# Performance work log

Measured on AMD Instinct MI355X. Metric: run time of the kernel, lower is better.

Reference implementation:

```python
import jax, jax.numpy as jnp
import numpy as np

T, N, M, B = 512, 512, 256, 256

def setup_inputs() -> dict:
    key = jax.random.key(0)
    ks = jax.random.split(key, 6)
    h_t = jax.random.normal(ks[0], (1, B, M), dtype=jnp.float32)
    s_t = jax.random.normal(ks[1], (1, B, M), dtype=jnp.float32)
    data = jax.random.normal(ks[2], (B, T, N), dtype=jnp.float32)
    # torch Linear weight layout: (out_features, in_features)
    W_e = jax.random.normal(ks[3], (T, 2 * M), dtype=jnp.float32) / np.sqrt(2 * M)
    U_e = jax.random.normal(ks[4], (T, T), dtype=jnp.float32) / np.sqrt(T)
    v_e = jax.random.normal(ks[5], (1, T), dtype=jnp.float32) / np.sqrt(T)
    return {"h_t": h_t, "s_t": s_t, "data": data, "W_e": W_e, "U_e": U_e, "v_e": v_e}

def reference(h_t, s_t, data, W_e, U_e, v_e):
    # h_t, s_t: (1, B, m) -> (B, 2m); query is identical across the n repeats,
    # so project once and broadcast instead of materializing (B, n, 2m).
    query = jnp.concatenate([h_t[0], s_t[0]], axis=-1)          # (B, 2m)
    wq = query @ W_e.T                                          # (B, T)
    ud = jnp.einsum('btn,st->bns', data, U_e)                   # (B, n, T)
    alpha = jnp.tanh(wq[:, None, :] + ud)                       # (B, n, T)
    scores = jnp.einsum('bnt,t->bn', alpha, v_e[0])             # (B, n)
    attn = jax.nn.softmax(scores, axis=-1)[:, None, :]          # (B, 1, n)
    return attn
```

## Files before the change

### kernel.cpp

```cpp
#include <hip/hip_runtime.h>
#include <hip/hip_bf16.h>
#include <cmath>

#define T_DIM 512
#define N_DIM 512
#define M_DIM 256
#define B_DIM 256

typedef __bf16 bf16x8 __attribute__((ext_vector_type(8)));
typedef float  f32x4  __attribute__((ext_vector_type(4)));
typedef unsigned int u32;

__device__ __forceinline__ void gload16(const __bf16* g, __bf16* l) {
    __builtin_amdgcn_global_load_lds(
        (const __attribute__((address_space(1))) void*)g,
        (__attribute__((address_space(3))) void*)l, 16, 0, 0);
}

__device__ __forceinline__ int bkey(int r) { return ((r >> 3) ^ (r >> 1)) & 3; }

__device__ __forceinline__ float ftanh(float x) {
    return 1.f - 2.f / (__expf(2.f * x) + 1.f);
}

__global__ __launch_bounds__(256) void uconv_kernel(
    const float* __restrict__ U, __bf16* __restrict__ Uh)
{
    const int i = (blockIdx.x * 256 + threadIdx.x) * 2;
    float2 v = *(const float2*)(U + i);
    Uh[i]   = (__bf16)v.x;
    Uh[i+1] = (__bf16)v.y;
}

__global__ __launch_bounds__(256) void wq_kernel(
    const float* __restrict__ h_t, const float* __restrict__ s_t,
    const float* __restrict__ W_e, float* __restrict__ wq)
{
    __shared__ float q[2 * M_DIM];
    const int b = blockIdx.x;
    const int tid = threadIdx.x;
    q[tid]         = h_t[(size_t)b * M_DIM + tid];
    q[M_DIM + tid] = s_t[(size_t)b * M_DIM + tid];
    __syncthreads();
    for (int tt = tid; tt < T_DIM; tt += 256) {
        const float4* wrow = (const float4*)(W_e + (size_t)tt * (2 * M_DIM));
        float acc = 0.f;
        #pragma unroll 4
        for (int k4 = 0; k4 < (2 * M_DIM) / 4; ++k4) {
            float4 w = wrow[k4];
            acc += q[4*k4+0] * w.x + q[4*k4+1] * w.y
                 + q[4*k4+2] * w.z + q[4*k4+3] * w.w;
        }
        wq[(size_t)b * T_DIM + tt] = acc;
    }
}

__global__ __launch_bounds__(256, 2) void fused8_kernel(
    const float* __restrict__ data, const __bf16* __restrict__ Uh,
    const float* __restrict__ v_e, const float* __restrict__ wq,
    float* __restrict__ partial)
{
    __shared__ __align__(16) __bf16 As[2][128 * 32];
    __shared__ __align__(16) __bf16 Bs[2][256 * 32];
    __shared__ float sc[128];

    const int wg    = blockIdx.x;
    const int xcd   = wg & 7;
    const int local = wg >> 3;
    const int sh    = local & 1;
    const int q     = xcd + 8 * (local >> 1);
    const int bgrp  = q >> 2;
    const int nb    = q & 3;

    const int tid  = threadIdx.x;
    const int lane = tid & 63;
    const int wid  = tid >> 6;
    const int wm   = wid >> 1;
    const int wn   = wid & 1;

    if (tid < 128) sc[tid] = 0.f;

    f32x4 acc[4][8];
    const f32x4 zero = {0.f, 0.f, 0.f, 0.f};
    #pragma unroll
    for (int i = 0; i < 4; ++i)
        #pragma unroll
        for (int j = 0; j < 8; ++j)
            acc[i][j] = zero;

    const int rp = tid >> 4;
    const int cg = tid & 15;
    const int n0 = cg * 8;

    const float* Apan = data + ((size_t)bgrp * 4 * T_DIM) * N_DIM + nb * 128 + n0;

    const __bf16* Bb = Uh + (size_t)(sh * 256) * T_DIM;
    const int r0   = tid >> 2;
    const int keyB = bkey(r0);
    const int ce   = (((tid & 3) ^ keyB) * 8);

    const int fr = lane & 15;
    const int kb = (lane >> 4) * 8;

    int aoff[4];
    #pragma unroll
    for (int mi = 0; mi < 4; ++mi) {
        const int row = wm * 64 + mi * 16 + fr;
        aoff[mi] = row * 32 + (kb ^ (bkey(row) << 3));
    }
    int boff[8];
    #pragma unroll
    for (int ni = 0; ni < 8; ++ni) {
        const int row = wn * 128 + ni * 16 + fr;
        boff[ni] = row * 32 + (kb ^ (bkey(row) << 3));
    }

    float vev[8];
    #pragma unroll
    for (int ni = 0; ni < 8; ++ni)
        vev[ni] = v_e[sh * 256 + wn * 128 + ni * 16 + fr];
    const int g = lane >> 4;

    float4 pa0, pa1, pa2, pa3;
    {
        const float* s0 = Apan + (size_t)(2 * rp) * N_DIM;
        pa0 = *(const float4*)s0;
        pa1 = *(const float4*)(s0 + 4);
        pa2 = *(const float4*)(s0 + N_DIM);
        pa3 = *(const float4*)(s0 + N_DIM + 4);
    }
    #pragma unroll
    for (int i = 0; i < 4; ++i)
        gload16(Bb + (size_t)(i * 64 + r0) * T_DIM + ce, &Bs[0][tid * 8] + i * 64 * 32);
    {
        u32* As32 = (u32*)As[0];
        const float lo_[8] = {pa0.x, pa0.y, pa0.z, pa0.w, pa1.x, pa1.y, pa1.z, pa1.w};
        const float hi_[8] = {pa2.x, pa2.y, pa2.z, pa2.w, pa3.x, pa3.y, pa3.z, pa3.w};
        #pragma unroll
        for (int j = 0; j < 8; ++j) {
            __bf16 l = (__bf16)lo_[j];
            __bf16 h = (__bf16)hi_[j];
            u32 w = ((u32)__builtin_bit_cast(unsigned short, h) << 16)
                  |  (u32)__builtin_bit_cast(unsigned short, l);
            const int key = (cg ^ (j >> 1)) & 3;
            As32[(n0 + j) * 16 + (rp ^ (key << 2))] = w;
        }
    }
    {
        const float* sn = Apan + (size_t)(32 + 2 * rp) * N_DIM;
        pa0 = *(const float4*)sn;
        pa1 = *(const float4*)(sn + 4);
        pa2 = *(const float4*)(sn + N_DIM);
        pa3 = *(const float4*)(sn + N_DIM + 4);
    }
    __syncthreads();

    for (int t = 0; t < 64; ++t) {
        const int cur = t & 1;

        bf16x8 a[4], bv[8];
        #pragma unroll
        for (int mi = 0; mi < 4; ++mi)
            a[mi] = *(const bf16x8*)&As[cur][aoff[mi]];
        #pragma unroll
        for (int ni = 0; ni < 8; ++ni)
            bv[ni] = *(const bf16x8*)&Bs[cur][boff[ni]];

        if (t < 63) {
            const int nxt = cur ^ 1;
            const int kcol = ((t + 1) & 15) << 5;
            #pragma unroll
            for (int i = 0; i < 4; ++i)
                gload16(Bb + (size_t)(i * 64 + r0) * T_DIM + kcol + ce,
                        &Bs[nxt][tid * 8] + i * 64 * 32);
            u32* As32 = (u32*)As[nxt];
            const float lo_[8] = {pa0.x, pa0.y, pa0.z, pa0.w, pa1.x, pa1.y, pa1.z, pa1.w};
            const float hi_[8] = {pa2.x, pa2.y, pa2.z, pa2.w, pa3.x, pa3.y, pa3.z, pa3.w};
            #pragma unroll
            for (int j = 0; j < 8; ++j) {
                __bf16 l = (__bf16)lo_[j];
                __bf16 h = (__bf16)hi_[j];
                u32 w = ((u32)__builtin_bit_cast(unsigned short, h) << 16)
                      |  (u32)__builtin_bit_cast(unsigned short, l);
                const int key = (cg ^ (j >> 1)) & 3;
                As32[(n0 + j) * 16 + (rp ^ (key << 2))] = w;
            }
            if (t < 62) {
                const float* sn = Apan + (size_t)(32 * (t + 2) + 2 * rp) * N_DIM;
                pa0 = *(const float4*)sn;
                pa1 = *(const float4*)(sn + 4);
                pa2 = *(const float4*)(sn + N_DIM);
                pa3 = *(const float4*)(sn + N_DIM + 4);
            }
        }

        __builtin_amdgcn_s_setprio(1);
        #pragma unroll
        for (int mi = 0; mi < 4; ++mi)
            #pragma unroll
            for (int ni = 0; ni < 8; ++ni)
                acc[mi][ni] = __builtin_amdgcn_mfma_f32_16x16x32_bf16(a[mi], bv[ni], acc[mi][ni], 0, 0, 0);
        __builtin_amdgcn_s_setprio(0);

        __syncthreads();

        if ((t & 15) == 15) {
            const int b = bgrp * 4 + (t >> 4);
            float wqv[8];
            #pragma unroll
            for (int ni = 0; ni < 8; ++ni)
                wqv[ni] = wq[(size_t)b * T_DIM + sh * 256 + wn * 128 + ni * 16 + fr];
            #pragma unroll
            for (int mi = 0; mi < 4; ++mi) {
                #pragma unroll
                for (int rg = 0; rg < 4; ++rg) {
                    float part = 0.f;
                    #pragma unroll
                    for (int ni = 0; ni < 8; ++ni)
                        part += vev[ni] * ftanh(wqv[ni] + acc[mi][ni][rg]);
                    part += __shfl_xor(part, 1);
                    part += __shfl_xor(part, 2);
                    part += __shfl_xor(part, 4);
                    part += __shfl_xor(part, 8);
                    if (fr == 0)
                        atomicAdd(&sc[wm * 64 + mi * 16 + 4 * g + rg], part);
                }
            }
            __syncthreads();
            if (tid < 128)
                partial[((size_t)b * 2 + sh) * N_DIM + nb * 128 + tid] = sc[tid];
            if (t < 63) {
                if (tid < 128) sc[tid] = 0.f;
                #pragma unroll
                for (int i = 0; i < 4; ++i)
                    #pragma unroll
                    for (int j = 0; j < 8; ++j)
                        acc[i][j] = zero;
            }
        }
    }
}

__global__ __launch_bounds__(512) void softmax_kernel(
    const float* __restrict__ partial, float* __restrict__ out)
{
    const int b = blockIdx.x;
    const int n = threadIdx.x;
    const float* p = partial + (size_t)b * 2 * N_DIM;
    float s = p[n] + p[N_DIM + n];

    float m = s;
    #pragma unroll
    for (int off = 1; off < 64; off <<= 1)
        m = fmaxf(m, __shfl_xor(m, off));
    __shared__ float red[8];
    const int wv = n >> 6;
    if ((n & 63) == 0) red[wv] = m;
    __syncthreads();
    float bm = red[0];
    #pragma unroll
    for (int i = 1; i < 8; ++i) bm = fmaxf(bm, red[i]);

    float e = expf(s - bm);
    float t = e;
    #pragma unroll
    for (int off = 1; off < 64; off <<= 1)
        t += __shfl_xor(t, off);
    __syncthreads();
    if ((n & 63) == 0) red[wv] = t;
    __syncthreads();
    float tot = 0.f;
    #pragma unroll
    for (int i = 0; i < 8; ++i) tot += red[i];

    out[(size_t)b * N_DIM + n] = e / tot;
}

extern "C" void kernel_launch(void* const* d_in, const int* in_sizes, int n_in,
                              void* d_out, int out_size, void* d_ws, size_t ws_size,
                              hipStream_t stream) {
    const float* h_t  = (const float*)d_in[0];
    const float* s_t  = (const float*)d_in[1];
    const float* data = (const float*)d_in[2];
    const float* W_e  = (const float*)d_in[3];
    const float* U_e  = (const float*)d_in[4];
    const float* v_e  = (const float*)d_in[5];
    float* out = (float*)d_out;

    const size_t wq_elems      = (size_t)B_DIM * T_DIM;
    const size_t partial_elems = (size_t)B_DIM * 2 * N_DIM;
    const size_t u_elems       = (size_t)T_DIM * T_DIM;

    float* wq      = (float*)d_ws;
    float* partial = wq + wq_elems;
    __bf16* Uh     = (__bf16*)(partial + partial_elems);

    wq_kernel<<<B_DIM, 256, 0, stream>>>(h_t, s_t, W_e, wq);
    uconv_kernel<<<(int)(u_elems / 512), 256, 0, stream>>>(U_e, Uh);
    fused8_kernel<<<512, 256, 0, stream>>>(data, Uh, v_e, wq, partial);
    softmax_kernel<<<B_DIM, 512, 0, stream>>>(partial, out);
}
```

Measured before the change: 164.7 us.

## Merge T-halves into one 512-thread block to load each data tile once

Each block now computes all 512 T columns with 8 waves instead of splitting T across two blocks, so each data tile is read from global memory and converted to bf16 only once. Per-wave score partials go to separate shared slots and are summed without atomics, and the softmax reads a single score row. In exchange the grid is halved to 256 blocks and LDS use per block doubles, which lowers the number of waves available to hide latency.

After: 163.5 us. About the same (-0.7%).

```diff
diff --git a/kernel.cpp b/kernel.cpp
--- a/kernel.cpp
+++ b/kernel.cpp
@@ -55,30 +55,24 @@
     }
 }
 
-__global__ __launch_bounds__(256, 2) void fused8_kernel(
+__global__ __launch_bounds__(512, 2) void fused9_kernel(
     const float* __restrict__ data, const __bf16* __restrict__ Uh,
     const float* __restrict__ v_e, const float* __restrict__ wq,
-    float* __restrict__ partial)
+    float* __restrict__ scores)
 {
     __shared__ __align__(16) __bf16 As[2][128 * 32];
-    __shared__ __align__(16) __bf16 Bs[2][256 * 32];
-    __shared__ float sc[128];
-
-    const int wg    = blockIdx.x;
-    const int xcd   = wg & 7;
-    const int local = wg >> 3;
-    const int sh    = local & 1;
-    const int q     = xcd + 8 * (local >> 1);
-    const int bgrp  = q >> 2;
-    const int nb    = q & 3;
+    __shared__ __align__(16) __bf16 Bs[2][512 * 32];
+    __shared__ float sc2[4][128];
+
+    const int wg   = blockIdx.x;
+    const int bgrp = wg >> 2;
+    const int nb   = wg & 3;
 
     const int tid  = threadIdx.x;
     const int lane = tid & 63;
     const int wid  = tid >> 6;
-    const int wm   = wid >> 1;
-    const int wn   = wid & 1;
-
-    if (tid < 128) sc[tid] = 0.f;
+    const int wm   = wid >> 2;
+    const int wn   = wid & 3;
 
     f32x4 acc[4][8];
     const f32x4 zero = {0.f, 0.f, 0.f, 0.f};
@@ -88,13 +82,13 @@
         for (int j = 0; j < 8; ++j)
             acc[i][j] = zero;
 
-    const int rp = tid >> 4;
-    const int cg = tid & 15;
-    const int n0 = cg * 8;
+    const int rp = tid >> 5;
+    const int nq = tid & 31;
+    const int n0 = nq * 4;
 
     const float* Apan = data + ((size_t)bgrp * 4 * T_DIM) * N_DIM + nb * 128 + n0;
 
-    const __bf16* Bb = Uh + (size_t)(sh * 256) * T_DIM;
+    const __bf16* Bb = Uh;
     const int r0   = tid >> 2;
     const int keyB = bkey(r0);
     const int ce   = (((tid & 3) ^ keyB) * 8);
@@ -118,40 +112,37 @@
     float vev[8];
     #pragma unroll
     for (int ni = 0; ni < 8; ++ni)
-        vev[ni] = v_e[sh * 256 + wn * 128 + ni * 16 + fr];
+        vev[ni] = v_e[wn * 128 + ni * 16 + fr];
     const int g = lane >> 4;
 
-    float4 pa0, pa1, pa2, pa3;
+    float4 pa0, pa1;
     {
         const float* s0 = Apan + (size_t)(2 * rp) * N_DIM;
         pa0 = *(const float4*)s0;
-        pa1 = *(const float4*)(s0 + 4);
-        pa2 = *(const float4*)(s0 + N_DIM);
-        pa3 = *(const float4*)(s0 + N_DIM + 4);
+        pa1 = *(const float4*)(s0 + N_DIM);
     }
     #pragma unroll
     for (int i = 0; i < 4; ++i)
-        gload16(Bb + (size_t)(i * 64 + r0) * T_DIM + ce, &Bs[0][tid * 8] + i * 64 * 32);
+        gload16(Bb + (size_t)(i * 128 + r0) * T_DIM + ce,
+                &Bs[0][0] + (size_t)i * 128 * 32 + tid * 8);
     {
         u32* As32 = (u32*)As[0];
-        const float lo_[8] = {pa0.x, pa0.y, pa0.z, pa0.w, pa1.x, pa1.y, pa1.z, pa1.w};
-        const float hi_[8] = {pa2.x, pa2.y, pa2.z, pa2.w, pa3.x, pa3.y, pa3.z, pa3.w};
-        #pragma unroll
-        for (int j = 0; j < 8; ++j) {
+        const float lo_[4] = {pa0.x, pa0.y, pa0.z, pa0.w};
+        const float hi_[4] = {pa1.x, pa1.y, pa1.z, pa1.w};
+        #pragma unroll
+        for (int j = 0; j < 4; ++j) {
             __bf16 l = (__bf16)lo_[j];
             __bf16 h = (__bf16)hi_[j];
             u32 w = ((u32)__builtin_bit_cast(unsigned short, h) << 16)
                   |  (u32)__builtin_bit_cast(unsigned short, l);
-            const int key = (cg ^ (j >> 1)) & 3;
+            const int key = bkey(n0 + j);
             As32[(n0 + j) * 16 + (rp ^ (key << 2))] = w;
         }
     }
     {
         const float* sn = Apan + (size_t)(32 + 2 * rp) * N_DIM;
         pa0 = *(const float4*)sn;
-        pa1 = *(const float4*)(sn + 4);
-        pa2 = *(const float4*)(sn + N_DIM);
-        pa3 = *(const float4*)(sn + N_DIM + 4);
+        pa1 = *(const float4*)(sn + N_DIM);
     }
     __syncthreads();
 
@@ -171,26 +162,24 @@
             const int kcol = ((t + 1) & 15) << 5;
             #pragma unroll
             for (int i = 0; i < 4; ++i)
-                gload16(Bb + (size_t)(i * 64 + r0) * T_DIM + kcol + ce,
-                        &Bs[nxt][tid * 8] + i * 64 * 32);
+                gload16(Bb + (size_t)(i * 128 + r0) * T_DIM + kcol + ce,
+                        &Bs[nxt][0] + (size_t)i * 128 * 32 + tid * 8);
             u32* As32 = (u32*)As[nxt];
-            const float lo_[8] = {pa0.x, pa0.y, pa0.z, pa0.w, pa1.x, pa1.y, pa1.z, pa1.w};
-            const float hi_[8] = {pa2.x, pa2.y, pa2.z, pa2.w, pa3.x, pa3.y, pa3.z, pa3.w};
-            #pragma unroll
-            for (int j = 0; j < 8; ++j) {
+            const float lo_[4] = {pa0.x, pa0.y, pa0.z, pa0.w};
+            const float hi_[4] = {pa1.x, pa1.y, pa1.z, pa1.w};
+            #pragma unroll
+            for (int j = 0; j < 4; ++j) {
                 __bf16 l = (__bf16)lo_[j];
                 __bf16 h = (__bf16)hi_[j];
                 u32 w = ((u32)__builtin_bit_cast(unsigned short, h) << 16)
                       |  (u32)__builtin_bit_cast(unsigned short, l);
-                const int key = (cg ^ (j >> 1)) & 3;
+                const int key = bkey(n0 + j);
                 As32[(n0 + j) * 16 + (rp ^ (key << 2))] = w;
             }
             if (t < 62) {
                 const float* sn = Apan + (size_t)(32 * (t + 2) + 2 * rp) * N_DIM;
                 pa0 = *(const float4*)sn;
-                pa1 = *(const float4*)(sn + 4);
-                pa2 = *(const float4*)(sn + N_DIM);
-                pa3 = *(const float4*)(sn + N_DIM + 4);
+                pa1 = *(const float4*)(sn + N_DIM);
             }
         }
 
@@ -209,7 +198,7 @@
             float wqv[8];
             #pragma unroll
             for (int ni = 0; ni < 8; ++ni)
-                wqv[ni] = wq[(size_t)b * T_DIM + sh * 256 + wn * 128 + ni * 16 + fr];
+                wqv[ni] = wq[(size_t)b * T_DIM + wn * 128 + ni * 16 + fr];
             #pragma unroll
             for (int mi = 0; mi < 4; ++mi) {
                 #pragma unroll
@@ -223,14 +212,15 @@
                     part += __shfl_xor(part, 4);
                     part += __shfl_xor(part, 8);
                     if (fr == 0)
-                        atomicAdd(&sc[wm * 64 + mi * 16 + 4 * g + rg], part);
+                        sc2[wn][wm * 64 + mi * 16 + 4 * g + rg] = part;
                 }
             }
             __syncthreads();
-            if (tid < 128)
-                partial[((size_t)b * 2 + sh) * N_DIM + nb * 128 + tid] = sc[tid];
+            if (tid < 128) {
+                const float s = sc2[0][tid] + sc2[1][tid] + sc2[2][tid] + sc2[3][tid];
+                scores[(size_t)b * N_DIM + nb * 128 + tid] = s;
+            }
             if (t < 63) {
-                if (tid < 128) sc[tid] = 0.f;
                 #pragma unroll
                 for (int i = 0; i < 4; ++i)
                     #pragma unroll
@@ -242,12 +232,11 @@
 }
 
 __global__ __launch_bounds__(512) void softmax_kernel(
-    const float* __restrict__ partial, float* __restrict__ out)
+    const float* __restrict__ scores, float* __restrict__ out)
 {
     const int b = blockIdx.x;
     const int n = threadIdx.x;
-    const float* p = partial + (size_t)b * 2 * N_DIM;
-    float s = p[n] + p[N_DIM + n];
+    float s = scores[(size_t)b * N_DIM + n];
 
     float m = s;
     #pragma unroll
@@ -287,16 +276,16 @@
     const float* v_e  = (const float*)d_in[5];
     float* out = (float*)d_out;
 
-    const size_t wq_elems      = (size_t)B_DIM * T_DIM;
-    const size_t partial_elems = (size_t)B_DIM * 2 * N_DIM;
-    const size_t u_elems       = (size_t)T_DIM * T_DIM;
+    const size_t wq_elems     = (size_t)B_DIM * T_DIM;
+    const size_t score_elems  = (size_t)B_DIM * N_DIM;
+    const size_t u_elems      = (size_t)T_DIM * T_DIM;
 
     float* wq      = (float*)d_ws;
-    float* partial = wq + wq_elems;
-    __bf16* Uh     = (__bf16*)(partial + partial_elems);
+    float* scores  = wq + wq_elems;
+    __bf16* Uh     = (__bf16*)(scores + score_elems);
 
     wq_kernel<<<B_DIM, 256, 0, stream>>>(h_t, s_t, W_e, wq);
     uconv_kernel<<<(int)(u_elems / 512), 256, 0, stream>>>(U_e, Uh);
-    fused8_kernel<<<512, 256, 0, stream>>>(data, Uh, v_e, wq, partial);
-    softmax_kernel<<<B_DIM, 512, 0, stream>>>(partial, out);
-}
+    fused9_kernel<<<256, 512, 0, stream>>>(data, Uh, v_e, wq, scores);
+    softmax_kernel<<<B_DIM, 512, 0, stream>>>(scores, out);
+}
```

## Split T output dimension into four quarters and double the grid

Applied to the files above, without the earlier changes.

Each workgroup now covers 128 of the T columns instead of 256, halving the accumulator tile and B shared-memory buffer. The grid grows to 1024 workgroups and launch bounds allow 3 per CU, aiming for more occupancy and better latency hiding. The LDS atomics are replaced with per-wave-column slots that are summed, and softmax now reduces four partials. The cost is that each data tile (fp32 to bf16 conversion plus global reads) is done twice as often, across four workgroups instead of two.

Result: slower. 213.4 us (+29.6%).

```diff
diff --git a/kernel.cpp b/kernel.cpp
--- a/kernel.cpp
+++ b/kernel.cpp
@@ -55,22 +55,22 @@
     }
 }
 
-__global__ __launch_bounds__(256, 2) void fused8_kernel(
+__global__ __launch_bounds__(256, 3) void fused10_kernel(
     const float* __restrict__ data, const __bf16* __restrict__ Uh,
     const float* __restrict__ v_e, const float* __restrict__ wq,
     float* __restrict__ partial)
 {
     __shared__ __align__(16) __bf16 As[2][128 * 32];
-    __shared__ __align__(16) __bf16 Bs[2][256 * 32];
-    __shared__ float sc[128];
-
-    const int wg    = blockIdx.x;
-    const int xcd   = wg & 7;
-    const int local = wg >> 3;
-    const int sh    = local & 1;
-    const int q     = xcd + 8 * (local >> 1);
-    const int bgrp  = q >> 2;
-    const int nb    = q & 3;
+    __shared__ __align__(16) __bf16 Bs[2][128 * 32];
+    __shared__ float sc2[2][128];
+
+    const int wg  = blockIdx.x;
+    const int xcd = wg & 7;
+    const int idx = wg >> 3;
+    const int sq  = idx & 3;
+    const int p   = xcd + 8 * (idx >> 2);
+    const int bgrp = p >> 2;
+    const int nb   = p & 3;
 
     const int tid  = threadIdx.x;
     const int lane = tid & 63;
@@ -78,26 +78,22 @@
     const int wm   = wid >> 1;
     const int wn   = wid & 1;
 
-    if (tid < 128) sc[tid] = 0.f;
-
-    f32x4 acc[4][8];
+    f32x4 acc[4][4];
     const f32x4 zero = {0.f, 0.f, 0.f, 0.f};
     #pragma unroll
     for (int i = 0; i < 4; ++i)
         #pragma unroll
-        for (int j = 0; j < 8; ++j)
+        for (int j = 0; j < 4; ++j)
             acc[i][j] = zero;
 
     const int rp = tid >> 4;
     const int cg = tid & 15;
     const int n0 = cg * 8;
-
     const float* Apan = data + ((size_t)bgrp * 4 * T_DIM) * N_DIM + nb * 128 + n0;
 
-    const __bf16* Bb = Uh + (size_t)(sh * 256) * T_DIM;
-    const int r0   = tid >> 2;
-    const int keyB = bkey(r0);
-    const int ce   = (((tid & 3) ^ keyB) * 8);
+    const __bf16* Bb = Uh + (size_t)(sq * 128) * T_DIM;
+    const int r0 = tid >> 2;
+    const int ce = (((tid & 3) ^ bkey(r0)) * 8);
 
     const int fr = lane & 15;
     const int kb = (lane >> 4) * 8;
@@ -108,17 +104,17 @@
         const int row = wm * 64 + mi * 16 + fr;
         aoff[mi] = row * 32 + (kb ^ (bkey(row) << 3));
     }
-    int boff[8];
-    #pragma unroll
-    for (int ni = 0; ni < 8; ++ni) {
-        const int row = wn * 128 + ni * 16 + fr;
+    int boff[4];
+    #pragma unroll
+    for (int ni = 0; ni < 4; ++ni) {
+        const int row = wn * 64 + ni * 16 + fr;
         boff[ni] = row * 32 + (kb ^ (bkey(row) << 3));
     }
 
-    float vev[8];
-    #pragma unroll
-    for (int ni = 0; ni < 8; ++ni)
-        vev[ni] = v_e[sh * 256 + wn * 128 + ni * 16 + fr];
+    float vev[4];
+    #pragma unroll
+    for (int ni = 0; ni < 4; ++ni)
+        vev[ni] = v_e[sq * 128 + wn * 64 + ni * 16 + fr];
     const int g = lane >> 4;
 
     float4 pa0, pa1, pa2, pa3;
@@ -129,9 +125,8 @@
         pa2 = *(const float4*)(s0 + N_DIM);
         pa3 = *(const float4*)(s0 + N_DIM + 4);
     }
-    #pragma unroll
-    for (int i = 0; i < 4; ++i)
-        gload16(Bb + (size_t)(i * 64 + r0) * T_DIM + ce, &Bs[0][tid * 8] + i * 64 * 32);
+    gload16(Bb + (size_t)r0 * T_DIM + ce,        &Bs[0][tid * 8]);
+    gload16(Bb + (size_t)(r0 + 64) * T_DIM + ce, &Bs[0][tid * 8] + 64 * 32);
     {
         u32* As32 = (u32*)As[0];
         const float lo_[8] = {pa0.x, pa0.y, pa0.z, pa0.w, pa1.x, pa1.y, pa1.z, pa1.w};
@@ -158,21 +153,19 @@
     for (int t = 0; t < 64; ++t) {
         const int cur = t & 1;
 
-        bf16x8 a[4], bv[8];
+        bf16x8 a[4], bv[4];
         #pragma unroll
         for (int mi = 0; mi < 4; ++mi)
             a[mi] = *(const bf16x8*)&As[cur][aoff[mi]];
         #pragma unroll
-        for (int ni = 0; ni < 8; ++ni)
+        for (int ni = 0; ni < 4; ++ni)
             bv[ni] = *(const bf16x8*)&Bs[cur][boff[ni]];
 
         if (t < 63) {
             const int nxt = cur ^ 1;
             const int kcol = ((t + 1) & 15) << 5;
-            #pragma unroll
-            for (int i = 0; i < 4; ++i)
-                gload16(Bb + (size_t)(i * 64 + r0) * T_DIM + kcol + ce,
-                        &Bs[nxt][tid * 8] + i * 64 * 32);
+            gload16(Bb + (size_t)r0 * T_DIM + kcol + ce,        &Bs[nxt][tid * 8]);
+            gload16(Bb + (size_t)(r0 + 64) * T_DIM + kcol + ce, &Bs[nxt][tid * 8] + 64 * 32);
             u32* As32 = (u32*)As[nxt];
             const float lo_[8] = {pa0.x, pa0.y, pa0.z, pa0.w, pa1.x, pa1.y, pa1.z, pa1.w};
             const float hi_[8] = {pa2.x, pa2.y, pa2.z, pa2.w, pa3.x, pa3.y, pa3.z, pa3.w};
@@ -198,7 +191,7 @@
         #pragma unroll
         for (int mi = 0; mi < 4; ++mi)
             #pragma unroll
-            for (int ni = 0; ni < 8; ++ni)
+            for (int ni = 0; ni < 4; ++ni)
                 acc[mi][ni] = __builtin_amdgcn_mfma_f32_16x16x32_bf16(a[mi], bv[ni], acc[mi][ni], 0, 0, 0);
         __builtin_amdgcn_s_setprio(0);
 
@@ -206,35 +199,36 @@
 
         if ((t & 15) == 15) {
             const int b = bgrp * 4 + (t >> 4);
-            float wqv[8];
-            #pragma unroll
-            for (int ni = 0; ni < 8; ++ni)
-                wqv[ni] = wq[(size_t)b * T_DIM + sh * 256 + wn * 128 + ni * 16 + fr];
+            float wqv[4];
+            #pragma unroll
+            for (int ni = 0; ni < 4; ++ni)
+                wqv[ni] = wq[(size_t)b * T_DIM + sq * 128 + wn * 64 + ni * 16 + fr];
             #pragma unroll
             for (int mi = 0; mi < 4; ++mi) {
                 #pragma unroll
                 for (int rg = 0; rg < 4; ++rg) {
                     float part = 0.f;
                     #pragma unroll
-                    for (int ni = 0; ni < 8; ++ni)
+                    for (int ni = 0; ni < 4; ++ni)
                         part += vev[ni] * ftanh(wqv[ni] + acc[mi][ni][rg]);
                     part += __shfl_xor(part, 1);
                     part += __shfl_xor(part, 2);
                     part += __shfl_xor(part, 4);
                     part += __shfl_xor(part, 8);
                     if (fr == 0)
-                        atomicAdd(&sc[wm * 64 + mi * 16 + 4 * g + rg], part);
+                        sc2[wn][wm * 64 + mi * 16 + 4 * g + rg] = part;
                 }
             }
             __syncthreads();
-            if (tid < 128)
-                partial[((size_t)b * 2 + sh) * N_DIM + nb * 128 + tid] = sc[tid];
+            if (tid < 128) {
+                const float s = sc2[0][tid] + sc2[1][tid];
+                partial[((size_t)b * 4 + sq) * N_DIM + nb * 128 + tid] = s;
+            }
             if (t < 63) {
-                if (tid < 128) sc[tid] = 0.f;
                 #pragma unroll
                 for (int i = 0; i < 4; ++i)
                     #pragma unroll
-                    for (int j = 0; j < 8; ++j)
+                    for (int j = 0; j < 4; ++j)
                         acc[i][j] = zero;
             }
         }
@@ -246,8 +240,8 @@
 {
     const int b = blockIdx.x;
     const int n = threadIdx.x;
-    const float* p = partial + (size_t)b * 2 * N_DIM;
-    float s = p[n] + p[N_DIM + n];
+    const float* p = partial + (size_t)b * 4 * N_DIM;
+    float s = p[n] + p[N_DIM + n] + p[2 * N_DIM + n] + p[3 * N_DIM + n];
 
     float m = s;
     #pragma unroll
@@ -288,7 +282,7 @@
     float* out = (float*)d_out;
 
     const size_t wq_elems      = (size_t)B_DIM * T_DIM;
-    const size_t partial_elems = (size_t)B_DIM * 2 * N_DIM;
+    const size_t partial_elems = (size_t)B_DIM * 4 * N_DIM;
     const size_t u_elems       = (size_t)T_DIM * T_DIM;
 
     float* wq      = (float*)d_ws;
@@ -297,6 +291,6 @@
 
     wq_kernel<<<B_DIM, 256, 0, stream>>>(h_t, s_t, W_e, wq);
     uconv_kernel<<<(int)(u_elems / 512), 256, 0, stream>>>(U_e, Uh);
-    fused8_kernel<<<512, 256, 0, stream>>>(data, Uh, v_e, wq, partial);
+    fused10_kernel<<<1024, 256, 0, stream>>>(data, Uh, v_e, wq, partial);
     softmax_kernel<<<B_DIM, 512, 0, stream>>>(partial, out);
 }
```
